# Optimization experiments

Hardware: AMD Instinct MI355X
Metric: run time of the kernel (lower is better)

The kernel has to match this reference:

```python
import jax, jax.numpy as jnp
import numpy as np

VOCAB, DIM, H, T, B, OUT = 50000, 300, 100, 512, 256, 3

def setup_inputs() -> dict:
    key = jax.random.key(0)
    ks = jax.random.split(key, 20)
    s = 1.0 / np.sqrt(H)
    def u(k, shape):
        return jax.random.uniform(k, shape, jnp.float32, -s, s)
    inp = {
        'x': jax.random.randint(ks[0], (B, T), 0, VOCAB),
        'lengths': jnp.clip(jax.random.randint(ks[1], (B,), 0, T), 1, T),
        'emb': jax.random.normal(ks[2], (VOCAB, DIM), jnp.float32),
    }
    dims = [DIM, H, H]
    ki = 3
    for l in range(3):
        inp[f'w_ih{l}'] = u(ks[ki], (4 * H, dims[l])); ki += 1
        inp[f'w_hh{l}'] = u(ks[ki], (4 * H, H)); ki += 1
        inp[f'b_ih{l}'] = u(ks[ki], (4 * H,)); ki += 1
        inp[f'b_hh{l}'] = u(ks[ki], (4 * H,)); ki += 1
    inp['w_fc'] = u(ks[ki], (OUT, H)); ki += 1
    inp['b_fc'] = u(ks[ki], (OUT,))
    return inp

def _lstm_layer(inp, w_ih, w_hh, b_ih, b_hh, mask):
    # inp: [B,T,D], mask: [T,B,1] True where t < length
    xg = jnp.einsum('btd,gd->btg', inp, w_ih) + b_ih + b_hh  # [B,T,4H]
    h0 = jnp.zeros((inp.shape[0], H), inp.dtype)
    def step(carry, xs):
        h, c = carry
        xg_t, m = xs
        g = xg_t + h @ w_hh.T
        i, f, gg, o = jnp.split(g, 4, axis=-1)  # torch gate order i,f,g,o
        c_new = jax.nn.sigmoid(f) * c + jax.nn.sigmoid(i) * jnp.tanh(gg)
        h_new = jax.nn.sigmoid(o) * jnp.tanh(c_new)
        h = jnp.where(m, h_new, h)  # hold state past sequence end (packed-seq semantics)
        c = jnp.where(m, c_new, c)
        return (h, c), h
    (h_last, _), hs = jax.lax.scan(step, (h0, h0), (xg.transpose(1, 0, 2), mask))
    return hs.transpose(1, 0, 2), h_last

def reference(x, lengths, emb,
              w_ih0, w_hh0, b_ih0, b_hh0,
              w_ih1, w_hh1, b_ih1, b_hh1,
              w_ih2, w_hh2, b_ih2, b_hh2,
              w_fc, b_fc):
    e = emb[x]  # [B,T,DIM] embedding lookup (frozen table)
    mask = (jnp.arange(T)[:, None] < lengths[None, :])[:, :, None]  # [T,B,1]
    h = e
    params = [(w_ih0, w_hh0, b_ih0, b_hh0), (w_ih1, w_hh1, b_ih1, b_hh1), (w_ih2, w_hh2, b_ih2, b_hh2)]
    for (wi, wh, bi, bh) in params:
        h, h_last = _lstm_layer(h, wi, wh, bi, bh, mask)
    # dropout p=0.0 -> identity; final linear head
    return h_last @ w_fc.T + b_fc  # [B,OUT]
```

## Files before the change

### kernel.cpp

```cpp
#include <hip/hip_runtime.h>
#include <hip/hip_bf16.h>

#define T_STEPS 512
#define BATCH   256
#define HID     100
#define GATES   400
#define BT      (BATCH * T_STEPS)

__device__ __forceinline__ float sigm_f(float x) {
    return 1.f / (1.f + __expf(-x));
}

__device__ __forceinline__ float tanh_f(float x) {
    float ax = fabsf(x);
    float t  = __expf(-2.f * ax);
    float r  = (1.f - t) / (1.f + t);
    return copysignf(r, x);
}

__device__ __forceinline__ unsigned short bf_hi(float f) {
    unsigned u = __float_as_uint(f);
    return (unsigned short)((u + 0x7FFFu + ((u >> 16) & 1u)) >> 16);
}
__device__ __forceinline__ float bf_f(unsigned short s) {
    return __uint_as_float(((unsigned)s) << 16);
}

typedef short v8s __attribute__((ext_vector_type(8)));
typedef float v4f __attribute__((ext_vector_type(4)));

template <int K, int NK, bool GATHER>
__global__ __launch_bounds__(256) void xg_gemm(
    const float* __restrict__ A, const int* __restrict__ idx,
    const float* __restrict__ W, const float* __restrict__ b1,
    const float* __restrict__ b2, float* __restrict__ out)
{
    __shared__ unsigned short Ah[2][4096], Al[2][4096];
    __shared__ unsigned short Wh[2][4096], Wl[2][4096];
    __shared__ int idx_s[128];

    const int bid  = blockIdx.x;
    const int xcd  = bid & 7;
    const int rest = bid >> 3;
    const int ct   = rest & 3;
    const int rgrp = rest >> 2;
    const int row0 = (rgrp * 8 + xcd) * 128;
    const int col0 = ct * 128;

    const int tid  = threadIdx.x;
    const int lane = tid & 63;
    const int wave = tid >> 6;
    const int wm   = wave >> 1;
    const int wn   = wave & 1;
    const int lm   = lane & 15;
    const int lk   = lane >> 4;

    if (GATHER) {
        if (tid < 128) idx_s[tid] = idx[row0 + tid];
        __syncthreads();
    }

    const int sr = tid >> 1;
    const int sq = (tid & 1) * 4;
    const float* arowp = GATHER ? (A + (size_t)idx_s[sr] * K)
                                : (A + (size_t)(row0 + sr) * K);
    const int    wrow  = col0 + sr;
    const bool   wval  = (wrow < GATES);
    const float* wrowp = W + (size_t)wrow * K;

    auto stage = [&](int ks, int buf) {
        const int k0 = ks * 32;
#pragma unroll
        for (int u = 0; u < 4; ++u) {
            int q  = sq + u;
            int kb = k0 + q * 4;
            float4 va = make_float4(0.f, 0.f, 0.f, 0.f);
            float4 vw = make_float4(0.f, 0.f, 0.f, 0.f);
            if (kb < K) {
                va = *(const float4*)(arowp + kb);
                if (wval) vw = *(const float4*)(wrowp + kb);
            }
            int bo = sr * 64 + q * 8;
            int so = bo ^ (((bo >> 6) & 7) << 4);
            unsigned short h0 = bf_hi(va.x), h1 = bf_hi(va.y),
                           h2 = bf_hi(va.z), h3 = bf_hi(va.w);
            *(ushort4*)((char*)Ah[buf] + so) = make_ushort4(h0, h1, h2, h3);
            *(ushort4*)((char*)Al[buf] + so) = make_ushort4(
                bf_hi(va.x - bf_f(h0)), bf_hi(va.y - bf_f(h1)),
                bf_hi(va.z - bf_f(h2)), bf_hi(va.w - bf_f(h3)));
            h0 = bf_hi(vw.x); h1 = bf_hi(vw.y);
            h2 = bf_hi(vw.z); h3 = bf_hi(vw.w);
            *(ushort4*)((char*)Wh[buf] + so) = make_ushort4(h0, h1, h2, h3);
            *(ushort4*)((char*)Wl[buf] + so) = make_ushort4(
                bf_hi(vw.x - bf_f(h0)), bf_hi(vw.y - bf_f(h1)),
                bf_hi(vw.z - bf_f(h2)), bf_hi(vw.w - bf_f(h3)));
        }
    };

    stage(0, 0);

    v4f acc[4][4];
#pragma unroll
    for (int fm = 0; fm < 4; ++fm)
#pragma unroll
        for (int fn = 0; fn < 4; ++fn)
            acc[fm][fn] = (v4f){0.f, 0.f, 0.f, 0.f};

#pragma unroll 1
    for (int ks = 0; ks < NK; ++ks) {
        __syncthreads();
        if (ks + 1 < NK) stage(ks + 1, (ks + 1) & 1);

        const int cur = ks & 1;
        v8s ah[4], al[4], bh[4], bl[4];
#pragma unroll
        for (int f = 0; f < 4; ++f) {
            int ra = (wm * 64 + f * 16 + lm) * 64 + lk * 16;
            ra ^= ((ra >> 6) & 7) << 4;
            ah[f] = *(const v8s*)((const char*)Ah[cur] + ra);
            al[f] = *(const v8s*)((const char*)Al[cur] + ra);
            int rb = (wn * 64 + f * 16 + lm) * 64 + lk * 16;
            rb ^= ((rb >> 6) & 7) << 4;
            bh[f] = *(const v8s*)((const char*)Wh[cur] + rb);
            bl[f] = *(const v8s*)((const char*)Wl[cur] + rb);
        }
#pragma unroll
        for (int fm = 0; fm < 4; ++fm) {
#pragma unroll
            for (int fn = 0; fn < 4; ++fn) {
                acc[fm][fn] = __builtin_amdgcn_mfma_f32_16x16x32_bf16(
                    ah[fm], bh[fn], acc[fm][fn], 0, 0, 0);
                acc[fm][fn] = __builtin_amdgcn_mfma_f32_16x16x32_bf16(
                    ah[fm], bl[fn], acc[fm][fn], 0, 0, 0);
                acc[fm][fn] = __builtin_amdgcn_mfma_f32_16x16x32_bf16(
                    al[fm], bh[fn], acc[fm][fn], 0, 0, 0);
            }
        }
    }

#pragma unroll
    for (int fn = 0; fn < 4; ++fn) {
        int col = col0 + wn * 64 + fn * 16 + lm;
        if (col < GATES) {
            float bias = b1[col] + b2[col];
#pragma unroll
            for (int fm = 0; fm < 4; ++fm) {
                v4f d = acc[fm][fn];
                int rbase = row0 + wm * 64 + fm * 16 + lk * 4;
#pragma unroll
                for (int p = 0; p < 4; ++p)
                    out[(size_t)(rbase + p) * GATES + col] = d[p] + bias;
            }
        }
    }
}

template <bool WRITE_ALL>
__global__ __launch_bounds__(448, 2) void lstm_recur(
    const float* __restrict__ xg,
    const float* __restrict__ w_hh,
    const int*   __restrict__ lengths,
    float* __restrict__ hs)
{
    const int b   = blockIdx.x;
    const int tid = threadIdx.x;
    const bool active = (tid < 400);
    const int j    = tid >> 2;
    const int gt   = tid & 3;

    __shared__ float xg_s[32 * GATES];
    __shared__ float h_s[2][112];
    __shared__ float h_hist[32 * HID];

    float w4[4][28];
    if (active) {
#pragma unroll
        for (int g = 0; g < 4; ++g) {
            const float* wr = w_hh + (size_t)(g * HID + j) * HID + gt * 25;
#pragma unroll
            for (int i = 0; i < 28; ++i)
                w4[g][i] = (i < 25) ? wr[i] : 0.f;
        }
    }
    for (int i = tid; i < 224; i += 448) ((float*)h_s)[i] = 0.f;

    float c_reg = 0.f, h_reg = 0.f;
    const int len = lengths[b];
    const float* xgb = xg + (size_t)b * T_STEPS * GATES;
    float*       hsb = hs + (size_t)b * T_STEPS * HID;

    const bool is0 = (gt == 0), is1 = (gt == 1), is2 = (gt == 2);
    const int  hoff = gt * 28;
    const int  seg  = (j / 25) * 28 + (j % 25);
    const int  xcol = gt * HID + j;

    for (int t = 0; t < T_STEPS; ++t) {
        if ((t & 31) == 0) {
            if (WRITE_ALL && t > 0) {
                const float4* s = (const float4*)h_hist;
                float4*       d = (float4*)(hsb + (size_t)(t - 32) * HID);
                for (int i = tid; i < 800; i += 448) d[i] = s[i];
            }
            const float4* src = (const float4*)(xgb + (size_t)t * GATES);
            float4*       dst = (float4*)xg_s;
            for (int i = tid; i < 3200; i += 448) dst[i] = src[i];
            __syncthreads();
        }

        float s0 = 0.f, s1 = 0.f, s2 = 0.f, s3 = 0.f;
        if (active) {
            const float* hb = h_s[t & 1] + hoff;
#pragma unroll
            for (int i = 0; i < 28; i += 4) {
                float4 h4 = *(const float4*)(hb + i);
                s0 += w4[0][i] * h4.x + w4[0][i+1] * h4.y +
                      w4[0][i+2] * h4.z + w4[0][i+3] * h4.w;
                s1 += w4[1][i] * h4.x + w4[1][i+1] * h4.y +
                      w4[1][i+2] * h4.z + w4[1][i+3] * h4.w;
                s2 += w4[2][i] * h4.x + w4[2][i+1] * h4.y +
                      w4[2][i+2] * h4.z + w4[2][i+3] * h4.w;
                s3 += w4[3][i] * h4.x + w4[3][i+1] * h4.y +
                      w4[3][i+2] * h4.z + w4[3][i+3] * h4.w;
            }
        }
        s0 += __shfl_xor(s0, 1); s0 += __shfl_xor(s0, 2);
        s1 += __shfl_xor(s1, 1); s1 += __shfl_xor(s1, 2);
        s2 += __shfl_xor(s2, 1); s2 += __shfl_xor(s2, 2);
        s3 += __shfl_xor(s3, 1); s3 += __shfl_xor(s3, 2);

        float sg = is0 ? s0 : is1 ? s1 : is2 ? s2 : s3;
        float pre = 0.f;
        if (active)
            pre = sg + xg_s[(t & 31) * GATES + xcol];

        float p0 = is2 ? tanh_f(pre) : sigm_f(pre);
        float p1 = __shfl_xor(p0, 1);
        float p2 = __shfl_xor(p0, 2);
        float p3 = __shfl_xor(p1, 2);
        float iv = is0 ? p0 : is1 ? p1 : is2 ? p2 : p3;
        float fv = is0 ? p1 : is1 ? p0 : is2 ? p3 : p2;
        float gv = is0 ? p2 : is1 ? p3 : is2 ? p0 : p1;
        float ov = is0 ? p3 : is1 ? p2 : is2 ? p1 : p0;

        float c_new = fv * c_reg + iv * gv;
        float h_new = ov * tanh_f(c_new);
        bool  m     = (t < len);
        c_reg = m ? c_new : c_reg;
        h_reg = m ? h_new : h_reg;

        if (active && gt == 0) {
            h_s[(t & 1) ^ 1][seg] = h_reg;
            if (WRITE_ALL) h_hist[(t & 31) * HID + j] = h_reg;
        }
        __syncthreads();
    }

    if (WRITE_ALL) {
        const float4* s = (const float4*)h_hist;
        float4*       d = (float4*)(hsb + (size_t)(T_STEPS - 32) * HID);
        for (int i = tid; i < 800; i += 448) d[i] = s[i];
    } else {
        if (active && gt == 0)
            hsb[(size_t)(T_STEPS - 1) * HID + j] = h_reg;
    }
}

__global__ __launch_bounds__(64) void fc_kernel(
    const float* __restrict__ hs, const float* __restrict__ w_fc,
    const float* __restrict__ b_fc, float* __restrict__ out)
{
    int tid = blockIdx.x * 64 + threadIdx.x;
    if (tid >= BATCH * 3) return;
    int b = tid / 3, o = tid % 3;
    const float* h = hs + ((size_t)b * T_STEPS + (T_STEPS - 1)) * HID;
    float acc = b_fc[o];
    for (int j = 0; j < HID; ++j) acc += h[j] * w_fc[o * HID + j];
    out[b * 3 + o] = acc;
}

extern "C" void kernel_launch(void* const* d_in, const int* in_sizes, int n_in,
                              void* d_out, int out_size, void* d_ws, size_t ws_size,
                              hipStream_t stream)
{
    const int*   x       = (const int*)  d_in[0];
    const int*   lengths = (const int*)  d_in[1];
    const float* emb     = (const float*)d_in[2];
    const float* w_ih0   = (const float*)d_in[3];
    const float* w_hh0   = (const float*)d_in[4];
    const float* b_ih0   = (const float*)d_in[5];
    const float* b_hh0   = (const float*)d_in[6];
    const float* w_ih1   = (const float*)d_in[7];
    const float* w_hh1   = (const float*)d_in[8];
    const float* b_ih1   = (const float*)d_in[9];
    const float* b_hh1   = (const float*)d_in[10];
    const float* w_ih2   = (const float*)d_in[11];
    const float* w_hh2   = (const float*)d_in[12];
    const float* b_ih2   = (const float*)d_in[13];
    const float* b_hh2   = (const float*)d_in[14];
    const float* w_fc    = (const float*)d_in[15];
    const float* b_fc    = (const float*)d_in[16];
    float* out = (float*)d_out;

    float* xg = (float*)d_ws;
    float* hs = xg + (size_t)BT * GATES;

    const int nblk = (BT / 128) * 4;

    xg_gemm<300, 10, true><<<nblk, 256, 0, stream>>>(emb, x, w_ih0, b_ih0, b_hh0, xg);
    lstm_recur<true><<<BATCH, 448, 0, stream>>>(xg, w_hh0, lengths, hs);

    xg_gemm<100, 4, false><<<nblk, 256, 0, stream>>>(hs, nullptr, w_ih1, b_ih1, b_hh1, xg);
    lstm_recur<true><<<BATCH, 448, 0, stream>>>(xg, w_hh1, lengths, hs);

    xg_gemm<100, 4, false><<<nblk, 256, 0, stream>>>(hs, nullptr, w_ih2, b_ih2, b_hh2, xg);
    lstm_recur<false><<<BATCH, 448, 0, stream>>>(xg, w_hh2, lengths, hs);

    fc_kernel<<<(BATCH * 3 + 63) / 64, 64, 0, stream>>>(hs, w_fc, b_fc, out);
}
```

Before: 2.069 ms.

## Run LSTM recurrence on bf16x3 MFMA with 16 sequences per block

Replaces the per-sequence scalar recurrence kernel with one where each block handles 16 batch rows. The recurrent matmul h@W_hh^T becomes split-bf16 (hi/lo, three products) MFMA ops, with W_hh held in registers as bf16 fragments. Gate pre-activations are prefetched from global two steps ahead, and hidden states are staged in shared memory and flushed every 8 steps. This trades the grid from 256 blocks down to 16, reducing parallelism across CUs, in exchange for matrix-core throughput and amortized weight loads; it also adds extra syncs per step.

```diff
diff --git a/kernel.cpp b/kernel.cpp
--- a/kernel.cpp
+++ b/kernel.cpp
@@ -6,6 +6,7 @@
 #define HID     100
 #define GATES   400
 #define BT      (BATCH * T_STEPS)
+#define NB      16
 
 __device__ __forceinline__ float sigm_f(float x) {
     return 1.f / (1.f + __expf(-x));
@@ -28,6 +29,19 @@
 
 typedef short v8s __attribute__((ext_vector_type(8)));
 typedef float v4f __attribute__((ext_vector_type(4)));
+
+__device__ __forceinline__ void split8(float4 a, float4 b, v8s& hi, v8s& lo) {
+    float f[8] = {a.x, a.y, a.z, a.w, b.x, b.y, b.z, b.w};
+    short h[8], l[8];
+#pragma unroll
+    for (int e = 0; e < 8; ++e) {
+        unsigned short hh = bf_hi(f[e]);
+        h[e] = (short)hh;
+        l[e] = (short)bf_hi(f[e] - bf_f(hh));
+    }
+    hi = (v8s){h[0], h[1], h[2], h[3], h[4], h[5], h[6], h[7]};
+    lo = (v8s){l[0], l[1], l[2], l[3], l[4], l[5], l[6], l[7]};
+}
 
 template <int K, int NK, bool GATHER>
 __global__ __launch_bounds__(256) void xg_gemm(
@@ -82,6 +96,8 @@
             }
             int bo = sr * 64 + q * 8;
             int so = bo ^ (((bo >> 6) & 7) << 4);
+            v8s hi, lo;
+            split8(va, make_float4(0,0,0,0), hi, lo);
             unsigned short h0 = bf_hi(va.x), h1 = bf_hi(va.y),
                            h2 = bf_hi(va.z), h3 = bf_hi(va.w);
             *(ushort4*)((char*)Ah[buf] + so) = make_ushort4(h0, h1, h2, h3);
@@ -156,112 +172,176 @@
 }
 
 template <bool WRITE_ALL>
-__global__ __launch_bounds__(448, 2) void lstm_recur(
+__global__ __launch_bounds__(512, 2) void lstm_recur_mfma(
     const float* __restrict__ xg,
     const float* __restrict__ w_hh,
     const int*   __restrict__ lengths,
     float* __restrict__ hs)
 {
-    const int b   = blockIdx.x;
-    const int tid = threadIdx.x;
-    const bool active = (tid < 400);
-    const int j    = tid >> 2;
-    const int gt   = tid & 3;
-
-    __shared__ float xg_s[32 * GATES];
-    __shared__ float h_s[2][112];
-    __shared__ float h_hist[32 * HID];
-
-    float w4[4][28];
-    if (active) {
-#pragma unroll
-        for (int g = 0; g < 4; ++g) {
-            const float* wr = w_hh + (size_t)(g * HID + j) * HID + gt * 25;
-#pragma unroll
-            for (int i = 0; i < 28; ++i)
-                w4[g][i] = (i < 25) ? wr[i] : 0.f;
-        }
-    }
-    for (int i = tid; i < 224; i += 448) ((float*)h_s)[i] = 0.f;
-
-    float c_reg = 0.f, h_reg = 0.f;
-    const int len = lengths[b];
-    const float* xgb = xg + (size_t)b * T_STEPS * GATES;
-    float*       hsb = hs + (size_t)b * T_STEPS * HID;
-
-    const bool is0 = (gt == 0), is1 = (gt == 1), is2 = (gt == 2);
-    const int  hoff = gt * 28;
-    const int  seg  = (j / 25) * 28 + (j % 25);
-    const int  xcol = gt * HID + j;
+    const int tid  = threadIdx.x;
+    const int lane = tid & 63;
+    const int w    = tid >> 6;
+    const int lm   = lane & 15;
+    const int lk   = lane >> 4;
+    const int b0   = blockIdx.x * NB;
+
+    __shared__ float pool[14336];
+    __shared__ float g_buf[NB][404];
+    __shared__ unsigned short H_hi[NB * 128], H_lo[NB * 128];
+    __shared__ int len_s[NB];
+
+    int  colI[4]; bool act[4], ist[4];
+#pragma unroll
+    for (int i = 0; i < 4; ++i) {
+        int ct = w + 8 * i;
+        act[i]  = (ct < 25);
+        colI[i] = ct * 16 + lm;
+        ist[i]  = act[i] && (colI[i] >= 200 && colI[i] < 300);
+    }
+
+    v8s wh[4][4], wl[4][4];
+    const v8s vz = (v8s){0,0,0,0,0,0,0,0};
+#pragma unroll
+    for (int i = 0; i < 4; ++i)
+#pragma unroll
+        for (int ks = 0; ks < 4; ++ks) { wh[i][ks] = vz; wl[i][ks] = vz; }
+
+    for (int c = 0; c < 4; ++c) {
+        for (int e = tid; e < 3584; e += 512) {
+            int colL = e >> 5, k4 = e & 31;
+            int col = c * 112 + colL, k = k4 * 4;
+            float4 v = make_float4(0.f, 0.f, 0.f, 0.f);
+            if (col < GATES && k < HID)
+                v = *(const float4*)(w_hh + (size_t)col * HID + k);
+            int byteo = (e << 4) ^ ((colL & 7) << 4);
+            *(float4*)((char*)pool + byteo) = v;
+        }
+        __syncthreads();
+#pragma unroll
+        for (int i = 0; i < 4; ++i) {
+            int ct = w + 8 * i;
+            if (act[i] && (ct / 7) == c) {
+                int colL = colI[i] - c * 112;
+#pragma unroll
+                for (int ks = 0; ks < 4; ++ks) {
+                    int base = colL * 128 + ks * 32 + lk * 8;
+                    int o1 = (base << 2) ^ ((colL & 7) << 4);
+                    int o2 = ((base + 4) << 2) ^ ((colL & 7) << 4);
+                    float4 u0 = *(const float4*)((const char*)pool + o1);
+                    float4 u1 = *(const float4*)((const char*)pool + o2);
+                    split8(u0, u1, wh[i][ks], wl[i][ks]);
+                }
+            }
+        }
+        __syncthreads();
+    }
+
+    for (int i2 = tid; i2 < NB * 128; i2 += 512) { H_hi[i2] = 0; H_lo[i2] = 0; }
+    if (tid < NB) len_s[tid] = lengths[b0 + tid];
+
+    int ub[4], uj[4]; bool uact[4];
+    float cc[4] = {0.f, 0.f, 0.f, 0.f}, hv[4] = {0.f, 0.f, 0.f, 0.f};
+#pragma unroll
+    for (int r = 0; r < 4; ++r) {
+        int u = tid + 512 * r;
+        uact[r] = (u < NB * HID);
+        int uu = uact[r] ? u : 0;
+        ub[r] = uu / HID; uj[r] = uu % HID;
+    }
+    __syncthreads();
+    int ulen[4];
+#pragma unroll
+    for (int r = 0; r < 4; ++r) ulen[r] = len_s[ub[r]];
+
+    size_t rowb[4];
+#pragma unroll
+    for (int p = 0; p < 4; ++p)
+        rowb[p] = ((size_t)(b0 + lk * 4 + p) * T_STEPS) * GATES;
+
+    float xpA[4][4], xpB[4][4];
+#pragma unroll
+    for (int i = 0; i < 4; ++i) if (act[i]) {
+#pragma unroll
+        for (int p = 0; p < 4; ++p) {
+            xpA[i][p] = xg[rowb[p] + colI[i]];
+            xpB[i][p] = xg[rowb[p] + GATES + colI[i]];
+        }
+    }
 
     for (int t = 0; t < T_STEPS; ++t) {
-        if ((t & 31) == 0) {
-            if (WRITE_ALL && t > 0) {
-                const float4* s = (const float4*)h_hist;
-                float4*       d = (float4*)(hsb + (size_t)(t - 32) * HID);
-                for (int i = tid; i < 800; i += 448) d[i] = s[i];
-            }
-            const float4* src = (const float4*)(xgb + (size_t)t * GATES);
-            float4*       dst = (float4*)xg_s;
-            for (int i = tid; i < 3200; i += 448) dst[i] = src[i];
-            __syncthreads();
-        }
-
-        float s0 = 0.f, s1 = 0.f, s2 = 0.f, s3 = 0.f;
-        if (active) {
-            const float* hb = h_s[t & 1] + hoff;
-#pragma unroll
-            for (int i = 0; i < 28; i += 4) {
-                float4 h4 = *(const float4*)(hb + i);
-                s0 += w4[0][i] * h4.x + w4[0][i+1] * h4.y +
-                      w4[0][i+2] * h4.z + w4[0][i+3] * h4.w;
-                s1 += w4[1][i] * h4.x + w4[1][i+1] * h4.y +
-                      w4[1][i+2] * h4.z + w4[1][i+3] * h4.w;
-                s2 += w4[2][i] * h4.x + w4[2][i+1] * h4.y +
-                      w4[2][i+2] * h4.z + w4[2][i+3] * h4.w;
-                s3 += w4[3][i] * h4.x + w4[3][i+1] * h4.y +
-                      w4[3][i+2] * h4.z + w4[3][i+3] * h4.w;
-            }
-        }
-        s0 += __shfl_xor(s0, 1); s0 += __shfl_xor(s0, 2);
-        s1 += __shfl_xor(s1, 1); s1 += __shfl_xor(s1, 2);
-        s2 += __shfl_xor(s2, 1); s2 += __shfl_xor(s2, 2);
-        s3 += __shfl_xor(s3, 1); s3 += __shfl_xor(s3, 2);
-
-        float sg = is0 ? s0 : is1 ? s1 : is2 ? s2 : s3;
-        float pre = 0.f;
-        if (active)
-            pre = sg + xg_s[(t & 31) * GATES + xcol];
-
-        float p0 = is2 ? tanh_f(pre) : sigm_f(pre);
-        float p1 = __shfl_xor(p0, 1);
-        float p2 = __shfl_xor(p0, 2);
-        float p3 = __shfl_xor(p1, 2);
-        float iv = is0 ? p0 : is1 ? p1 : is2 ? p2 : p3;
-        float fv = is0 ? p1 : is1 ? p0 : is2 ? p3 : p2;
-        float gv = is0 ? p2 : is1 ? p3 : is2 ? p0 : p1;
-        float ov = is0 ? p3 : is1 ? p2 : is2 ? p1 : p0;
-
-        float c_new = fv * c_reg + iv * gv;
-        float h_new = ov * tanh_f(c_new);
-        bool  m     = (t < len);
-        c_reg = m ? c_new : c_reg;
-        h_reg = m ? h_new : h_reg;
-
-        if (active && gt == 0) {
-            h_s[(t & 1) ^ 1][seg] = h_reg;
-            if (WRITE_ALL) h_hist[(t & 31) * HID + j] = h_reg;
-        }
-        __syncthreads();
-    }
-
-    if (WRITE_ALL) {
-        const float4* s = (const float4*)h_hist;
-        float4*       d = (float4*)(hsb + (size_t)(T_STEPS - 32) * HID);
-        for (int i = tid; i < 800; i += 448) d[i] = s[i];
-    } else {
-        if (active && gt == 0)
-            hsb[(size_t)(T_STEPS - 1) * HID + j] = h_reg;
+        v4f acc[4];
+#pragma unroll
+        for (int i = 0; i < 4; ++i) acc[i] = (v4f){0.f, 0.f, 0.f, 0.f};
+#pragma unroll
+        for (int ks = 0; ks < 4; ++ks) {
+            int ob = ((lm * 128 + ks * 32 + lk * 8) << 1) ^ ((lm & 7) << 4);
+            v8s ah = *(const v8s*)((const char*)H_hi + ob);
+            v8s al = *(const v8s*)((const char*)H_lo + ob);
+#pragma unroll
+            for (int i = 0; i < 4; ++i) if (act[i]) {
+                acc[i] = __builtin_amdgcn_mfma_f32_16x16x32_bf16(ah, wh[i][ks], acc[i], 0, 0, 0);
+                acc[i] = __builtin_amdgcn_mfma_f32_16x16x32_bf16(ah, wl[i][ks], acc[i], 0, 0, 0);
+                acc[i] = __builtin_amdgcn_mfma_f32_16x16x32_bf16(al, wh[i][ks], acc[i], 0, 0, 0);
+            }
+        }
+
+        auto cphase = [&](float (&XP)[4][4]) {
+#pragma unroll
+            for (int i = 0; i < 4; ++i) if (act[i]) {
+#pragma unroll
+                for (int p = 0; p < 4; ++p) {
+                    float pre = acc[i][p] + XP[i][p];
+                    float xx  = ist[i] ? pre + pre : pre;
+                    float s   = 1.f / (1.f + __expf(-xx));
+                    float a   = ist[i] ? s + s - 1.f : s;
+                    g_buf[lk * 4 + p][colI[i]] = a;
+                }
+                if (t + 2 < T_STEPS) {
+#pragma unroll
+                    for (int p = 0; p < 4; ++p)
+                        XP[i][p] = xg[rowb[p] + (size_t)(t + 2) * GATES + colI[i]];
+                }
+            }
+        };
+        if ((t & 1) == 0) cphase(xpA); else cphase(xpB);
+        __syncthreads();
+
+#pragma unroll
+        for (int r = 0; r < 4; ++r) if (uact[r]) {
+            float gi = g_buf[ub[r]][uj[r]];
+            float gf = g_buf[ub[r]][HID + uj[r]];
+            float gg = g_buf[ub[r]][2 * HID + uj[r]];
+            float go = g_buf[ub[r]][3 * HID + uj[r]];
+            float cn = gf * cc[r] + gi * gg;
+            float hn = go * tanh_f(cn);
+            bool  m  = (t < ulen[r]);
+            cc[r] = m ? cn : cc[r];
+            hv[r] = m ? hn : hv[r];
+            unsigned short hb = bf_hi(hv[r]);
+            unsigned short lb = bf_hi(hv[r] - bf_f(hb));
+            int ob = ((ub[r] * 128 + uj[r]) << 1) ^ ((ub[r] & 7) << 4);
+            *(unsigned short*)((char*)H_hi + ob) = hb;
+            *(unsigned short*)((char*)H_lo + ob) = lb;
+            pool[(t & 7) * (NB * HID) + tid + 512 * r] = hv[r];
+        }
+        __syncthreads();
+
+        if (WRITE_ALL && (t & 7) == 7) {
+            int tb = t - 7;
+            for (int e2 = tid; e2 < 3200; e2 += 512) {
+                float4 v = ((const float4*)pool)[e2];
+                int ts  = e2 / 400;
+                int rem = e2 % 400;
+                int bb = rem / 25, j4 = rem % 25;
+                *(float4*)(hs + ((size_t)(b0 + bb) * T_STEPS + (tb + ts)) * HID + j4 * 4) = v;
+            }
+        }
+    }
+
+    if (!WRITE_ALL) {
+#pragma unroll
+        for (int r = 0; r < 4; ++r) if (uact[r])
+            hs[((size_t)(b0 + ub[r]) * T_STEPS + (T_STEPS - 1)) * HID + uj[r]] = hv[r];
     }
 }
 
@@ -307,13 +387,13 @@
     const int nblk = (BT / 128) * 4;
 
     xg_gemm<300, 10, true><<<nblk, 256, 0, stream>>>(emb, x, w_ih0, b_ih0, b_hh0, xg);
-    lstm_recur<true><<<BATCH, 448, 0, stream>>>(xg, w_hh0, lengths, hs);
+    lstm_recur_mfma<true><<<BATCH / NB, 512, 0, stream>>>(xg, w_hh0, lengths, hs);
 
     xg_gemm<100, 4, false><<<nblk, 256, 0, stream>>>(hs, nullptr, w_ih1, b_ih1, b_hh1, xg);
-    lstm_recur<true><<<BATCH, 448, 0, stream>>>(xg, w_hh1, lengths, hs);
+    lstm_recur_mfma<true><<<BATCH / NB, 512, 0, stream>>>(xg, w_hh1, lengths, hs);
 
     xg_gemm<100, 4, false><<<nblk, 256, 0, stream>>>(hs, nullptr, w_ih2, b_ih2, b_hh2, xg);
-    lstm_recur<false><<<BATCH, 448, 0, stream>>>(xg, w_hh2, lengths, hs);
+    lstm_recur_mfma<false><<<BATCH / NB, 512, 0, stream>>>(xg, w_hh2, lengths, hs);
 
     fc_kernel<<<(BATCH * 3 + 63) / 64, 64, 0, stream>>>(hs, w_fc, b_fc, out);
 }
```

Result: slower. 4.426 ms (+114.0%).
